# Performance work log

Hardware: AMD Instinct MI355X
Metric: run time of the kernel (lower is better)

Reference implementation:

```python
import jax, jax.numpy as jnp
import numpy as np

EMB_DIM = 1024
HEAD_SIZE = 128
B, T = 8, 2048


def setup_inputs() -> dict:
    key = jax.random.key(0)
    kx, kk, kq, kv = jax.random.split(key, 4)
    x = jax.random.normal(kx, (B, T, EMB_DIM), dtype=jnp.float32)
    # torch nn.Linear(emb_dim, head_size, bias=False): weight [head_size, emb_dim], y = x @ W.T
    # store transposed as [emb_dim, head_size] for direct matmul
    s = 1.0 / np.sqrt(EMB_DIM)
    Wk = jax.random.uniform(kk, (EMB_DIM, HEAD_SIZE), dtype=jnp.float32, minval=-s, maxval=s)
    Wq = jax.random.uniform(kq, (EMB_DIM, HEAD_SIZE), dtype=jnp.float32, minval=-s, maxval=s)
    Wv = jax.random.uniform(kv, (EMB_DIM, HEAD_SIZE), dtype=jnp.float32, minval=-s, maxval=s)
    return {"x": x, "Wk": Wk, "Wq": Wq, "Wv": Wv}


def reference(x, Wk, Wq, Wv):
    Bb, Tt, C = x.shape
    k = jnp.einsum('btc,ch->bth', x, Wk)
    q = jnp.einsum('btc,ch->bth', x, Wq)
    v = jnp.einsum('btc,ch->bth', x, Wv)
    # NOTE: original computes k @ q^T (not q @ k^T) and scales by C**-0.5 (C = emb_dim)
    wei = jnp.einsum('bih,bjh->bij', k, q) * (C ** -0.5)  # [B, T, T]
    causal = jnp.tril(jnp.ones((Tt, Tt), dtype=bool))
    wei = jnp.where(causal, wei, -jnp.inf)
    wei = jax.nn.softmax(wei, axis=-1)
    out = jnp.einsum('bij,bjh->bih', wei, v)  # [B, T, head_size]
    return out
```

## Files before the change

kernel.cpp:

```cpp
#include <hip/hip_runtime.h>
#include <hip/hip_bf16.h>
#include <stdint.h>

#define Bn 8
#define Tn 2048
#define Cn 1024
#define Hn 128

typedef __attribute__((ext_vector_type(8))) short short8;
typedef __attribute__((ext_vector_type(4))) short short4v;
typedef __attribute__((ext_vector_type(4))) float f32x4;
typedef __attribute__((ext_vector_type(4))) int int4v;

static __device__ __forceinline__ unsigned short f2bf(float f) {
    union { float f; unsigned int u; } v; v.f = f;
    return (unsigned short)((v.u + 0x7FFFu + ((v.u >> 16) & 1u)) >> 16);
}
static __device__ __forceinline__ float bf2f(unsigned short h) {
    union { unsigned int u; float f; } v; v.u = ((unsigned int)h) << 16;
    return v.f;
}

static __device__ __forceinline__ short8 cvt8(f32x4 a, f32x4 b) {
    union { unsigned int u[4]; short8 s; } r;
    asm("v_cvt_pk_bf16_f32 %0, %1, %2" : "=v"(r.u[0]) : "v"(a[0]), "v"(a[1]));
    asm("v_cvt_pk_bf16_f32 %0, %1, %2" : "=v"(r.u[1]) : "v"(a[2]), "v"(a[3]));
    asm("v_cvt_pk_bf16_f32 %0, %1, %2" : "=v"(r.u[2]) : "v"(b[0]), "v"(b[1]));
    asm("v_cvt_pk_bf16_f32 %0, %1, %2" : "=v"(r.u[3]) : "v"(b[2]), "v"(b[3]));
    return r.s;
}

static __device__ __forceinline__ void async16(const void* g, void* l) {
    __builtin_amdgcn_global_load_lds(
        (const __attribute__((address_space(1))) unsigned int*)g,
        (__attribute__((address_space(3))) unsigned int*)l,
        16, 0, 0);
}

#define KSCALE 0.04508422f

#define BASE_BYTES (3u * Bn * Tn * Hn * 2u + 3u * Hn * Cn * 2u)
#define SLOT_SH 2080
#define NBLK_FA 576
#define UPB_FA 72
#define CCHUNK 8

__global__ __launch_bounds__(256) void wt_prep(const float* __restrict__ Wk,
                                               const float* __restrict__ Wq,
                                               const float* __restrict__ Wv,
                                               unsigned short* __restrict__ WT) {
    int z = blockIdx.y;
    const float* W = (z == 0) ? Wk : (z == 1) ? Wq : Wv;
    unsigned short* wt = WT + (size_t)z * Hn * Cn;
    int o = blockIdx.x * 256 + threadIdx.x;
    int d = o >> 10;
    int k = o & (Cn - 1);
    wt[o] = f2bf(W[k * Hn + d]);
}

__global__ __launch_bounds__(256) void proj7(const float* __restrict__ x,
                                             const unsigned short* __restrict__ WTb,
                                             unsigned short* __restrict__ Kb,
                                             unsigned short* __restrict__ Qb,
                                             unsigned short* __restrict__ VT) {
    __shared__ __align__(16) unsigned short Bsm[2][128 * 64];
    __shared__ __align__(16) unsigned short Asm[2][64 * 64];
    int tid = threadIdx.x;
    int lane = tid & 63, w = tid >> 6;
    int lr = lane & 15, lg = lane >> 4;
    int wm = w >> 1, wn = w & 1;

    int u = ((int)(blockIdx.x & 7)) * 96 + ((int)blockIdx.x >> 3);
    int rg = u / 3, cg = u - rg * 3;
    int r0 = rg * 64;
    const unsigned short* WTz = WTb + (size_t)cg * Hn * Cn;

    int brow_in = lane >> 3;
    int bslot = (lane & 7) ^ brow_in;
    const unsigned short* bsrc[4];
    #pragma unroll
    for (int i = 0; i < 4; ++i) {
        int ch = w * 4 + i;
        bsrc[i] = WTz + (size_t)(ch * 8 + brow_in) * Cn + bslot * 8;
    }

    int ar_s = tid >> 2;
    int ah = tid & 3;
    const float* axp = x + (size_t)(r0 + ar_s) * Cn + ah * 16;
    int asw = (ar_s & 7) << 4;
    unsigned int awb0 = ar_s * 128 + ((ah * 32) ^ asw);
    unsigned int awb1 = ar_s * 128 + ((ah * 32 + 16) ^ asw);

    f32x4 a_r[4];
    auto LOADA = [&](int k0) {
        #pragma unroll
        for (int i = 0; i < 4; ++i)
            a_r[i] = *(const f32x4*)(axp + k0 + i * 4);
    };
    auto STAGEB = [&](int bb, int k0) {
        #pragma unroll
        for (int i = 0; i < 4; ++i)
            async16(bsrc[i] + k0, &Bsm[bb][(w * 4 + i) * 512]);
    };
    auto WRITEA = [&](int bb) {
        short8 w0 = cvt8(a_r[0], a_r[1]);
        short8 w1 = cvt8(a_r[2], a_r[3]);
        char* base = (char*)&Asm[bb][0];
        *(short8*)(base + awb0) = w0;
        *(short8*)(base + awb1) = w1;
    };

    f32x4 acc[2][4] = {};
    LOADA(0);
    STAGEB(0, 0);
    WRITEA(0);
    __syncthreads();
    int cur = 0;
    for (int ks = 0; ks < 16; ++ks) {
        if (ks < 15) {
            LOADA((ks + 1) * 64);
            STAGEB(cur ^ 1, (ks + 1) * 64);
        }
        const char* ab = (const char*)&Asm[cur][0];
        const char* bbp = (const char*)&Bsm[cur][0];
        #pragma unroll
        for (int kk = 0; kk < 2; ++kk) {
            short8 af[2], bf[4];
            #pragma unroll
            for (int m = 0; m < 2; ++m) {
                int row = wm * 32 + m * 16 + lr;
                af[m] = *(const short8*)(ab + row * 128 + ((kk * 64 + lg * 16) ^ ((row & 7) << 4)));
            }
            #pragma unroll
            for (int c = 0; c < 4; ++c) {
                int row = wn * 64 + c * 16 + lr;
                bf[c] = *(const short8*)(bbp + row * 128 + ((kk * 64 + lg * 16) ^ ((row & 7) << 4)));
            }
            #pragma unroll
            for (int m = 0; m < 2; ++m)
                #pragma unroll
                for (int c = 0; c < 4; ++c)
                    acc[m][c] = __builtin_amdgcn_mfma_f32_16x16x32_bf16(af[m], bf[c], acc[m][c], 0, 0, 0);
        }
        if (ks < 15) WRITEA(cur ^ 1);
        __syncthreads();
        cur ^= 1;
    }

    if (cg == 2) {
        int bb = r0 >> 11;
        int tb = r0 & 2047;
        #pragma unroll
        for (int m = 0; m < 2; ++m)
            #pragma unroll
            for (int c = 0; c < 4; ++c) {
                int d = wn * 64 + c * 16 + lr;
                int t = tb + wm * 32 + m * 16 + lg * 4;
                short4v pv;
                pv[0] = (short)f2bf(acc[m][c][0]);
                pv[1] = (short)f2bf(acc[m][c][1]);
                pv[2] = (short)f2bf(acc[m][c][2]);
                pv[3] = (short)f2bf(acc[m][c][3]);
                *(short4v*)(VT + ((size_t)(bb * Hn + d) << 11) + t) = pv;
            }
    } else {
        unsigned short* outp = (cg == 0) ? Kb : Qb;
        float sc = (cg == 0) ? KSCALE : 1.0f;
        #pragma unroll
        for (int m = 0; m < 2; ++m)
            #pragma unroll
            for (int c = 0; c < 4; ++c) {
                int d = wn * 64 + c * 16 + lr;
                #pragma unroll
                for (int r = 0; r < 4; ++r) {
                    int i = r0 + wm * 32 + m * 16 + lg * 4 + r;
                    outp[(size_t)i * Hn + d] = f2bf(acc[m][c][r] * sc);
                }
            }
    }
}

__global__ __launch_bounds__(512) void fattn8(const unsigned short* __restrict__ Kb,
                                              const unsigned short* __restrict__ Qb,
                                              const unsigned short* __restrict__ VT,
                                              unsigned short* __restrict__ accP) {
    __shared__ __align__(16) unsigned short Ksm[2][32 * 128];
    __shared__ __align__(16) unsigned short Vsm[2][128 * 32];
    __shared__ __align__(16) unsigned short pbuf[8][16][48];
    int tid = threadIdx.x, lane = tid & 63, w = tid >> 6;
    int lr = lane & 15, lg = lane >> 4;

    int cpx = gridDim.x >> 3;
    int u = ((int)blockIdx.x & 7) * cpx + ((int)blockIdx.x >> 3);
    int b = u / UPB_FA, rem = u - b * UPB_FA;
    int g = 0, p = 0;
    for (;;) {
        int P = (4 * g + 4 + CCHUNK - 1) / CCHUNK;
        if (rem < P) { p = rem; break; }
        rem -= P; ++g;
    }
    int nt = 4 * g + 4;
    int P = (nt + CCHUNK - 1) / CCHUNK;
    int q = nt / P, r = nt % P;
    int begin = p * q + (p < r ? p : r);
    int size = q + (p < r ? 1 : 0);

    int i0 = g * 128 + w * 16;
    int tmax = (i0 + 15) >> 5;
    const unsigned short* kb = Kb + (size_t)b * Tn * Hn;
    const unsigned short* qb = Qb + (size_t)b * Tn * Hn;
    const unsigned short* vt = VT + (size_t)b * Hn * Tn;

    short8 kf[4];
    #pragma unroll
    for (int kk = 0; kk < 4; ++kk)
        kf[kk] = *(const short8*)(kb + (size_t)(i0 + lr) * Hn + kk * 32 + lg * 8);

    int krow = tid >> 4, kcol = (tid & 15) * 8;
    int vrow = tid >> 2, vcol = (tid & 3) * 8;
    int4v kreg, vreg;
    auto LOADT = [&](int tt) {
        int j0 = tt * 32;
        kreg = *(const int4v*)(qb + (size_t)(j0 + krow) * Hn + kcol);
        vreg = *(const int4v*)(vt + (size_t)vrow * Tn + j0 + vcol);
    };
    auto WRITET = [&](int bb) {
        *(int4v*)((char*)&Ksm[bb][0] + krow * 256 + ((kcol * 2) ^ ((krow & 7) << 4))) = kreg;
        *(int4v*)((char*)&Vsm[bb][0] + vrow * 64 + vcol * 2) = vreg;
    };

    f32x4 acc[8] = {};
    float ssum[4] = {0.f, 0.f, 0.f, 0.f};

    LOADT(begin);
    WRITET(0);
    __syncthreads();
    int cur = 0;
    for (int ti = 0; ti < size; ++ti) {
        int tt = begin + ti;
        if (ti + 1 < size) LOADT(tt + 1);
        if (tt <= tmax) {
            int j0 = tt * 32;
            const char* kbp = (const char*)&Ksm[cur][0];
            const char* vbp = (const char*)&Vsm[cur][0];
            f32x4 sa0 = {}, sa1 = {};
            #pragma unroll
            for (int kk = 0; kk < 4; ++kk) {
                int row = lr;
                short8 qf = *(const short8*)(kbp + row * 256 + (((kk * 64) + lg * 16) ^ ((row & 7) << 4)));
                sa0 = __builtin_amdgcn_mfma_f32_16x16x32_bf16(kf[kk], qf, sa0, 0, 0, 0);
            }
            #pragma unroll
            for (int kk = 0; kk < 4; ++kk) {
                int row = 16 + lr;
                short8 qf = *(const short8*)(kbp + row * 256 + (((kk * 64) + lg * 16) ^ ((row & 7) << 4)));
                sa1 = __builtin_amdgcn_mfma_f32_16x16x32_bf16(kf[kk], qf, sa1, 0, 0, 0);
            }
            bool needmask = (j0 + 31 > i0);
            #pragma unroll
            for (int rr = 0; rr < 4; ++rr) {
                float v0 = sa0[rr], v1 = sa1[rr];
                if (needmask) {
                    int i = i0 + lg * 4 + rr;
                    if (j0 + lr > i)      v0 = -1e30f;
                    if (j0 + 16 + lr > i) v1 = -1e30f;
                }
                float p0 = __builtin_amdgcn_exp2f(v0);
                float p1 = __builtin_amdgcn_exp2f(v1);
                ssum[rr] += p0 + p1;
                pbuf[w][lg * 4 + rr][lr] = f2bf(p0);
                pbuf[w][lg * 4 + rr][16 + lr] = f2bf(p1);
            }
            short8 pf = *(const short8*)(&pbuf[w][lr][lg * 8]);
            #pragma unroll
            for (int n = 0; n < 8; ++n) {
                int row = n * 16 + lr;
                short8 vf = *(const short8*)(vbp + row * 64 + lg * 16);
                acc[n] = __builtin_amdgcn_mfma_f32_16x16x32_bf16(pf, vf, acc[n], 0, 0, 0);
            }
        }
        if (ti + 1 < size) WRITET(cur ^ 1);
        __syncthreads();
        cur ^= 1;
    }

    unsigned short* dst = accP + (size_t)u * 8 * SLOT_SH + (size_t)w * SLOT_SH;
    #pragma unroll
    for (int n = 0; n < 8; ++n) {
        short4v pv;
        pv[0] = (short)f2bf(acc[n][0]);
        pv[1] = (short)f2bf(acc[n][1]);
        pv[2] = (short)f2bf(acc[n][2]);
        pv[3] = (short)f2bf(acc[n][3]);
        *(short4v*)(dst + n * 256 + lane * 4) = pv;
    }
    #pragma unroll
    for (int rr = 0; rr < 4; ++rr) {
        float s = ssum[rr];
        s += __shfl_xor(s, 1);
        s += __shfl_xor(s, 2);
        s += __shfl_xor(s, 4);
        s += __shfl_xor(s, 8);
        if (lr == 0) ((float*)(dst + 2048))[lg * 4 + rr] = s;
    }
}

__global__ __launch_bounds__(256) void combine3(const unsigned short* __restrict__ accP,
                                                float* __restrict__ out) {
    int cpx = gridDim.x >> 3;
    int bidx = ((int)blockIdx.x & 7) * cpx + ((int)blockIdx.x >> 3);
    int b = bidx >> 7, tile = bidx & 127;
    int g = tile >> 3, wq = tile & 7;
    int ub = b * UPB_FA;
    for (int gg = 0; gg < g; ++gg) ub += (4 * gg + 4 + CCHUNK - 1) / CCHUNK;
    int nt = 4 * g + 4;
    int P = (nt + CCHUNK - 1) / CCHUNK;

    int tid = threadIdx.x;
    int row = tid >> 4;
    int c8 = (tid & 15) * 8;

    const unsigned short* base = accP + ((size_t)ub * 8 + wq) * SLOT_SH;
    const size_t pstr = (size_t)8 * SLOT_SH;
    float den = 0.f;
    for (int pp = 0; pp < P; ++pp) den += ((const float*)(base + pp * pstr + 2048))[row];
    float inv = 1.0f / den;

    int lgg = row >> 2, r4 = row & 3;
    float ov[8];
    #pragma unroll
    for (int cc = 0; cc < 8; ++cc) {
        int col = c8 + cc;
        int n = col >> 4, lrr = col & 15;
        int flat = n * 256 + (lgg * 16 + lrr) * 4 + r4;
        float s = 0.f;
        for (int pp = 0; pp < P; ++pp) s += bf2f(base[pp * pstr + flat]);
        ov[cc] = s * inv;
    }
    float* op = out + ((size_t)(b * Tn + tile * 16 + row)) * Hn + c8;
    *(f32x4*)op       = f32x4{ov[0], ov[1], ov[2], ov[3]};
    *(f32x4*)(op + 4) = f32x4{ov[4], ov[5], ov[6], ov[7]};
}

__global__ __launch_bounds__(256) void attn(const unsigned short* __restrict__ Kb,
                                            const unsigned short* __restrict__ Qb,
                                            const unsigned short* __restrict__ VT,
                                            float* __restrict__ out) {
    __shared__ unsigned short pbuf[4][16][32];
    __shared__ __align__(16) float accbuf[4][16][132];
    __shared__ float ssbuf[4][16];
    int lane = threadIdx.x & 63;
    int w = threadIdx.x >> 6;
    int b = blockIdx.y;
    int xb = blockIdx.x;
    int tile = (xb & 1) ? (127 - (xb >> 1)) : (xb >> 1);
    int i0 = tile * 16;
    int lr = lane & 15, lg = lane >> 4;

    const unsigned short* kb = Kb + (size_t)b * Tn * Hn;
    const unsigned short* qb = Qb + (size_t)b * Tn * Hn;
    const unsigned short* vt = VT + (size_t)b * Hn * Tn;

    short8 kf[4];
    #pragma unroll
    for (int kk = 0; kk < 4; ++kk)
        kf[kk] = *(const short8*)(kb + (size_t)(i0 + lr) * Hn + kk * 32 + lg * 8);

    f32x4 acc[8] = {};
    float ssum[4] = {0.f, 0.f, 0.f, 0.f};

    int nt = (i0 + 15) / 32 + 1;
    for (int tt = w; tt < nt; tt += 4) {
        int j0 = tt * 32;
        f32x4 sa0 = {}, sa1 = {};
        #pragma unroll
        for (int kk = 0; kk < 4; ++kk) {
            short8 q0 = *(const short8*)(qb + (size_t)(j0 + lr) * Hn + kk * 32 + lg * 8);
            sa0 = __builtin_amdgcn_mfma_f32_16x16x32_bf16(kf[kk], q0, sa0, 0, 0, 0);
        }
        #pragma unroll
        for (int kk = 0; kk < 4; ++kk) {
            short8 q1 = *(const short8*)(qb + (size_t)(j0 + 16 + lr) * Hn + kk * 32 + lg * 8);
            sa1 = __builtin_amdgcn_mfma_f32_16x16x32_bf16(kf[kk], q1, sa1, 0, 0, 0);
        }
        bool needmask = (j0 + 31 > i0);
        #pragma unroll
        for (int r = 0; r < 4; ++r) {
            float v0 = sa0[r], v1 = sa1[r];
            if (needmask) {
                int i = i0 + lg * 4 + r;
                if (j0 + lr > i)      v0 = -1e30f;
                if (j0 + 16 + lr > i) v1 = -1e30f;
            }
            float p0 = __builtin_amdgcn_exp2f(v0);
            float p1 = __builtin_amdgcn_exp2f(v1);
            ssum[r] += p0 + p1;
            pbuf[w][lg * 4 + r][lr] = f2bf(p0);
            pbuf[w][lg * 4 + r][16 + lr] = f2bf(p1);
        }
        short8 pf = *(const short8*)(&pbuf[w][lr][lg * 8]);
        #pragma unroll
        for (int n = 0; n < 8; ++n) {
            short8 vf = *(const short8*)(vt + (size_t)(n * 16 + lr) * Tn + j0 + lg * 8);
            acc[n] = __builtin_amdgcn_mfma_f32_16x16x32_bf16(pf, vf, acc[n], 0, 0, 0);
        }
    }

    #pragma unroll
    for (int r = 0; r < 4; ++r) {
        float s = ssum[r];
        s += __shfl_xor(s, 1);
        s += __shfl_xor(s, 2);
        s += __shfl_xor(s, 4);
        s += __shfl_xor(s, 8);
        if (lr == 0) ssbuf[w][lg * 4 + r] = s;
    }
    #pragma unroll
    for (int n = 0; n < 8; ++n)
        #pragma unroll
        for (int r = 0; r < 4; ++r)
            accbuf[w][lg * 4 + r][n * 16 + lr] = acc[n][r];
    __syncthreads();

    int row = threadIdx.x >> 5;
    int col = (threadIdx.x & 31) * 4;
    #pragma unroll
    for (int h = 0; h < 2; ++h) {
        int rr = row + h * 8;
        f32x4 s = *(const f32x4*)(&accbuf[0][rr][col]);
        #pragma unroll
        for (int ww = 1; ww < 4; ++ww) {
            f32x4 t = *(const f32x4*)(&accbuf[ww][rr][col]);
            s[0] += t[0]; s[1] += t[1]; s[2] += t[2]; s[3] += t[3];
        }
        float den = ssbuf[0][rr] + ssbuf[1][rr] + ssbuf[2][rr] + ssbuf[3][rr];
        float inv = 1.0f / den;
        s[0] *= inv; s[1] *= inv; s[2] *= inv; s[3] *= inv;
        *(f32x4*)(&out[((size_t)(b * Tn + i0 + rr)) * Hn + col]) = s;
    }
}

extern "C" void kernel_launch(void* const* d_in, const int* in_sizes, int n_in,
                              void* d_out, int out_size, void* d_ws, size_t ws_size,
                              hipStream_t stream) {
    const float* x  = (const float*)d_in[0];
    const float* Wk = (const float*)d_in[1];
    const float* Wq = (const float*)d_in[2];
    const float* Wv = (const float*)d_in[3];

    unsigned short* Kb = (unsigned short*)d_ws;
    unsigned short* Qb = Kb + (size_t)Bn * Tn * Hn;
    unsigned short* VT = Qb + (size_t)Bn * Tn * Hn;
    unsigned short* WT = VT + (size_t)Bn * Tn * Hn;
    unsigned short* accP = (unsigned short*)((char*)d_ws + BASE_BYTES);

    wt_prep<<<dim3(512, 3), 256, 0, stream>>>(Wk, Wq, Wv, WT);
    proj7<<<dim3(768), 256, 0, stream>>>(x, WT, Kb, Qb, VT);

    const size_t need = (size_t)BASE_BYTES + (size_t)NBLK_FA * 8 * SLOT_SH * 2;
    if (ws_size >= need) {
        fattn8<<<dim3(NBLK_FA), 512, 0, stream>>>(Kb, Qb, VT, accP);
        combine3<<<dim3(1024), 256, 0, stream>>>(accP, (float*)d_out);
    } else {
        attn<<<dim3(128, 8), 256, 0, stream>>>(Kb, Qb, VT, (float*)d_out);
    }
}
```

Baseline: 83.93 us.

## Deepen projection GEMM pipeline to three B stages with explicit vmcnt waits

Reworks the QKV projection kernel's K-loop from a double-buffered scheme to a deeper software pipeline. B tiles use a triple LDS buffer and A is prefetched two steps ahead into two register sets. Partial s_waitcnt vmcnt plus a raw barrier replace __syncthreads so that loads stay in flight across iterations. This aims to hide global-load latency in the projection, but it raises LDS use and register pressure and relies on hand-counted vmcnt values being correct.

```diff
diff --git a/kernel.cpp b/kernel.cpp
--- a/kernel.cpp
+++ b/kernel.cpp
@@ -58,12 +58,12 @@
     wt[o] = f2bf(W[k * Hn + d]);
 }
 
-__global__ __launch_bounds__(256) void proj7(const float* __restrict__ x,
+__global__ __launch_bounds__(256) void proj8(const float* __restrict__ x,
                                              const unsigned short* __restrict__ WTb,
                                              unsigned short* __restrict__ Kb,
                                              unsigned short* __restrict__ Qb,
                                              unsigned short* __restrict__ VT) {
-    __shared__ __align__(16) unsigned short Bsm[2][128 * 64];
+    __shared__ __align__(16) unsigned short Bsm[3][128 * 64];
     __shared__ __align__(16) unsigned short Asm[2][64 * 64];
     int tid = threadIdx.x;
     int lane = tid & 63, w = tid >> 6;
@@ -91,38 +91,42 @@
     unsigned int awb0 = ar_s * 128 + ((ah * 32) ^ asw);
     unsigned int awb1 = ar_s * 128 + ((ah * 32 + 16) ^ asw);
 
-    f32x4 a_r[4];
-    auto LOADA = [&](int k0) {
+    auto LOADA = [&](f32x4 (&d)[4], int k0) {
         #pragma unroll
         for (int i = 0; i < 4; ++i)
-            a_r[i] = *(const f32x4*)(axp + k0 + i * 4);
+            d[i] = *(const f32x4*)(axp + k0 + i * 4);
     };
     auto STAGEB = [&](int bb, int k0) {
         #pragma unroll
         for (int i = 0; i < 4; ++i)
             async16(bsrc[i] + k0, &Bsm[bb][(w * 4 + i) * 512]);
     };
-    auto WRITEA = [&](int bb) {
-        short8 w0 = cvt8(a_r[0], a_r[1]);
-        short8 w1 = cvt8(a_r[2], a_r[3]);
-        char* base = (char*)&Asm[bb][0];
+    auto WRITEA = [&](int ab, f32x4 (&d)[4]) {
+        short8 w0 = cvt8(d[0], d[1]);
+        short8 w1 = cvt8(d[2], d[3]);
+        char* base = (char*)&Asm[ab][0];
         *(short8*)(base + awb0) = w0;
         *(short8*)(base + awb1) = w1;
     };
 
     f32x4 acc[2][4] = {};
-    LOADA(0);
+    f32x4 A0[4], A1[4];
+
+    LOADA(A0, 0);
     STAGEB(0, 0);
-    WRITEA(0);
-    __syncthreads();
-    int cur = 0;
-    for (int ks = 0; ks < 16; ++ks) {
-        if (ks < 15) {
-            LOADA((ks + 1) * 64);
-            STAGEB(cur ^ 1, (ks + 1) * 64);
-        }
-        const char* ab = (const char*)&Asm[cur][0];
-        const char* bbp = (const char*)&Bsm[cur][0];
+    STAGEB(1, 64);
+    WRITEA(0, A0);
+    LOADA(A0, 64);
+    LOADA(A1, 128);
+
+    auto BODY = [&](int ks, f32x4 (&CUR)[4]) {
+        if (ks < 15) asm volatile("s_waitcnt vmcnt(8) lgkmcnt(0)" ::: "memory");
+        else         asm volatile("s_waitcnt vmcnt(0) lgkmcnt(0)" ::: "memory");
+        __builtin_amdgcn_s_barrier();
+        __builtin_amdgcn_sched_barrier(0);
+        if (ks + 2 <= 15) STAGEB((ks + 2) % 3, (ks + 2) * 64);
+        const char* ab = (const char*)&Asm[ks & 1][0];
+        const char* bbp = (const char*)&Bsm[ks % 3][0];
         #pragma unroll
         for (int kk = 0; kk < 2; ++kk) {
             short8 af[2], bf[4];
@@ -142,9 +146,13 @@
                 for (int c = 0; c < 4; ++c)
                     acc[m][c] = __builtin_amdgcn_mfma_f32_16x16x32_bf16(af[m], bf[c], acc[m][c], 0, 0, 0);
         }
-        if (ks < 15) WRITEA(cur ^ 1);
-        __syncthreads();
-        cur ^= 1;
+        if (ks + 1 <= 15) WRITEA((ks + 1) & 1, CUR);
+        if (ks + 3 <= 15) LOADA(CUR, (ks + 3) * 64);
+    };
+
+    for (int k2 = 0; k2 < 16; k2 += 2) {
+        BODY(k2, A0);
+        BODY(k2 + 1, A1);
     }
 
     if (cg == 2) {
@@ -455,7 +463,7 @@
     unsigned short* accP = (unsigned short*)((char*)d_ws + BASE_BYTES);
 
     wt_prep<<<dim3(512, 3), 256, 0, stream>>>(Wk, Wq, Wv, WT);
-    proj7<<<dim3(768), 256, 0, stream>>>(x, WT, Kb, Qb, VT);
+    proj8<<<dim3(768), 256, 0, stream>>>(x, WT, Kb, Qb, VT);
 
     const size_t need = (size_t)BASE_BYTES + (size_t)NBLK_FA * 8 * SLOT_SH * 2;
     if (ws_size >= need) {
```

Result: slower. 87.49 us (+4.2%).
